# Kernel tuning notes

Hardware: AMD Instinct MI355X
Metric: run time of the kernel (lower is better)

The kernel has to match this reference:

```python
import jax, jax.numpy as jnp
import numpy as np

BATCH, DIN, DSTATE, SEQLEN = 4, 2048, 16, 2048


def setup_inputs() -> dict:
    key = jax.random.key(0)
    ks = jax.random.split(key, 7)
    u = jax.random.normal(ks[0], (BATCH, DIN, SEQLEN), dtype=jnp.float32)
    # delta pre-softplus; moderate positive-ish values like Mamba dt_proj output
    delta = jax.random.uniform(ks[1], (BATCH, DIN, SEQLEN), dtype=jnp.float32, minval=-2.0, maxval=1.0)
    # A is negative in real Mamba (A = -exp(A_log)); keep recurrence stable
    A = -jnp.exp(jax.random.uniform(ks[2], (DIN, DSTATE), dtype=jnp.float32, minval=-1.0, maxval=1.0))
    B = jax.random.normal(ks[3], (BATCH, DSTATE, SEQLEN), dtype=jnp.float32)
    C = jax.random.normal(ks[4], (BATCH, DSTATE, SEQLEN), dtype=jnp.float32)
    D = jax.random.normal(ks[5], (DIN,), dtype=jnp.float32)
    z = jax.random.normal(ks[6], (BATCH, DIN, SEQLEN), dtype=jnp.float32)
    return {"u": u, "delta": delta, "A": A, "B": B, "C": C, "D": D, "z": z}


def reference(u, delta, A, B, C, D, z):
    """Mamba selective scan (selective_scan_ref semantics, delta_softplus=True).

    u, delta, z: (b, d, l); A: (d, n); B, C: (b, n, l); D: (d,).
    y_t = C_t . x_t + D*u_t, x_t = exp(dt_t*A)*x_{t-1} + dt_t*B_t*u_t,
    final y gated by SiLU(z).
    """
    dt = jax.nn.softplus(delta)                      # (b, d, l)

    def step(x, inp):
        dt_t, u_t, B_t, C_t = inp                    # (b,d) (b,d) (b,n) (b,n)
        dA = jnp.exp(dt_t[..., None] * A)            # (b, d, n)
        x = x * dA + (dt_t * u_t)[..., None] * B_t[:, None, :]
        y_t = jnp.einsum('bdn,bn->bd', x, C_t)
        return x, y_t

    xs = (jnp.moveaxis(dt, -1, 0),                   # (l, b, d)
          jnp.moveaxis(u, -1, 0),
          jnp.moveaxis(B, -1, 0),                    # (l, b, n)
          jnp.moveaxis(C, -1, 0))
    x0 = jnp.zeros((u.shape[0], u.shape[1], A.shape[1]), dtype=u.dtype)
    _, ys = jax.lax.scan(step, x0, xs)               # ys: (l, b, d)
    y = jnp.moveaxis(ys, 0, -1)                      # (b, d, l)
    y = y + D[None, :, None] * u
    y = y * (z * jax.nn.sigmoid(z))                  # SiLU gate
    return y
```

## Files before the change

kernel.cpp:

```cpp
#include <hip/hip_runtime.h>


#define BATCHSZ 4
#define DIN 2048
#define NSTATE 16
#define SEQ 2048
#define NCH (BATCHSZ * DIN)
#define NGRP (NCH / 256)
#define TT 16
#define ST 20
#define L2E 1.44269504f

__device__ __forceinline__ float softplus_f(float v) {
    float e = __builtin_amdgcn_exp2f(v * L2E);
    return 0.69314718f * __builtin_amdgcn_logf(1.0f + e);
}

__device__ __forceinline__ float silu_f(float v) {
    float s = __builtin_amdgcn_rcpf(1.0f + __builtin_amdgcn_exp2f(-v * L2E));
    return v * s;
}

__device__ __forceinline__ float comp4(const float4& f, int k) {
    return k == 0 ? f.x : k == 1 ? f.y : k == 2 ? f.z : f.w;
}

__device__ __forceinline__ void set4(float4& f, int k, float v) {
    if (k == 0) f.x = v; else if (k == 1) f.y = v; else if (k == 2) f.z = v; else f.w = v;
}


template<int NC>
__global__ __launch_bounds__(256, 3) void k_pass1(
        const float* __restrict__ u, const float* __restrict__ delta,
        const float* __restrict__ A, const float* __restrict__ Bm,
        float* __restrict__ ws) {
    constexpr int LC = SEQ / NC;
    constexpr int NT = LC / TT;
    __shared__ float Ub[256 * ST];
    __shared__ float Db[256 * ST];
    __shared__ float Bc[LC * 20];

    int tid = threadIdx.x;
    int g = blockIdx.x & (NGRP - 1);
    int c = blockIdx.x >> 5;
    int chBase = g << 8;
    int b = chBase >> 11;
    int bd = chBase + tid;
    int d = bd & (DIN - 1);

    float A2[NSTATE];
    {
        const float* Ar = A + (size_t)d * NSTATE;
        #pragma unroll
        for (int n = 0; n < NSTATE; ++n) A2[n] = Ar[n] * L2E;
    }

    const float* ug = u + (size_t)chBase * SEQ + (size_t)c * LC;
    const float* dg = delta + (size_t)chBase * SEQ + (size_t)c * LC;
    const float* Bg = Bm + (size_t)b * NSTATE * SEQ + (size_t)c * LC;

    #pragma unroll
    for (int i = 0; i < LC * NSTATE / 256; ++i) {
        int e = i * 256 + tid;
        int n = e / LC;
        int t = e % LC;
        Bc[t * 20 + n] = Bg[(size_t)n * SEQ + t];
    }

    float x[NSTATE];
    #pragma unroll
    for (int n = 0; n < NSTATE; ++n) x[n] = 0.0f;
    float S = 0.0f;

    float4 uvr[4], dvr[4];
    #pragma unroll
    for (int it = 0; it < 4; ++it) {
        int r = it * 64 + (tid >> 2), cq = (tid & 3) * 4;
        uvr[it] = *(const float4*)(ug + (size_t)r * SEQ + cq);
        dvr[it] = *(const float4*)(dg + (size_t)r * SEQ + cq);
    }

    for (int tile = 0; tile < NT; ++tile) {
        int tb = tile * TT;
        __syncthreads();
        #pragma unroll
        for (int it = 0; it < 4; ++it) {
            int r = it * 64 + (tid >> 2), cq = (tid & 3) * 4;
            *(float4*)(&Ub[r * ST + cq]) = uvr[it];
            *(float4*)(&Db[r * ST + cq]) = dvr[it];
        }
        __syncthreads();
        if (tile + 1 < NT) {
            #pragma unroll
            for (int it = 0; it < 4; ++it) {
                int r = it * 64 + (tid >> 2), cq = (tid & 3) * 4;
                uvr[it] = *(const float4*)(ug + (size_t)r * SEQ + tb + TT + cq);
                dvr[it] = *(const float4*)(dg + (size_t)r * SEQ + tb + TT + cq);
            }
        }
        #pragma unroll
        for (int t4 = 0; t4 < TT / 4; ++t4) {
            float4 u4 = *(const float4*)(&Ub[tid * ST + t4 * 4]);
            float4 d4 = *(const float4*)(&Db[tid * ST + t4 * 4]);
            #pragma unroll
            for (int k = 0; k < 4; ++k) {
                float dt = softplus_f(comp4(d4, k));
                S += dt;
                float du = dt * comp4(u4, k);
                int t = tb + t4 * 4 + k;
                const float4* Br = (const float4*)(&Bc[t * 20]);
                float bb[NSTATE];
                *(float4*)&bb[0] = Br[0]; *(float4*)&bb[4] = Br[1];
                *(float4*)&bb[8] = Br[2]; *(float4*)&bb[12] = Br[3];
                #pragma unroll
                for (int n = 0; n < NSTATE; ++n) {
                    float dA = __builtin_amdgcn_exp2f(A2[n] * dt);
                    x[n] = x[n] * dA + du * bb[n];
                }
            }
        }
    }

    float* wsq = ws;
    float* wsS = ws + (size_t)NSTATE * NC * NCH;
    #pragma unroll
    for (int n = 0; n < NSTATE; ++n) wsq[((size_t)n * NC + c) * NCH + bd] = x[n];
    wsS[(size_t)c * NCH + bd] = S;
}

template<int NC>
__global__ __launch_bounds__(256) void k_pass2(
        const float* __restrict__ A, float* __restrict__ ws) {
    int idx = blockIdx.x * 256 + threadIdx.x;
    int n = idx >> 13;
    int bd = idx & (NCH - 1);
    int d = bd & (DIN - 1);

    float A2 = A[(size_t)d * NSTATE + n] * L2E;
    float x = 0.0f;
    float* wsq = ws;
    float* wsS = ws + (size_t)NSTATE * NC * NCH;

    for (int c = 0; c < NC; ++c) {
        float S = wsS[(size_t)c * NCH + bd];
        float* p = wsq + ((size_t)n * NC + c) * NCH + bd;
        float q = *p;
        float P = __builtin_amdgcn_exp2f(A2 * S);
        *p = x;
        x = x * P + q;
    }
}

template<int NC>
__global__ __launch_bounds__(256, 3) void k_pass3(
        const float* __restrict__ u, const float* __restrict__ delta,
        const float* __restrict__ A, const float* __restrict__ Bm,
        const float* __restrict__ Cm, const float* __restrict__ Dv,
        const float* __restrict__ z, const float* __restrict__ ws,
        float* __restrict__ out) {
    constexpr int LC = SEQ / NC;
    constexpr int NT = LC / TT;
    __shared__ float Ub[256 * ST];
    __shared__ float Db[256 * ST];
    __shared__ float Bc[LC * 20];
    __shared__ float Cc[LC * 20];

    int tid = threadIdx.x;
    int g = blockIdx.x & (NGRP - 1);
    int c = blockIdx.x >> 5;
    int chBase = g << 8;
    int b = chBase >> 11;
    int bd = chBase + tid;
    int d = bd & (DIN - 1);

    float A2[NSTATE];
    {
        const float* Ar = A + (size_t)d * NSTATE;
        #pragma unroll
        for (int n = 0; n < NSTATE; ++n) A2[n] = Ar[n] * L2E;
    }

    const float* ug = u + (size_t)chBase * SEQ + (size_t)c * LC;
    const float* dg = delta + (size_t)chBase * SEQ + (size_t)c * LC;
    const float* zg = z + (size_t)chBase * SEQ + (size_t)c * LC;
    float* og = out + (size_t)chBase * SEQ + (size_t)c * LC;
    const float* Bg = Bm + (size_t)b * NSTATE * SEQ + (size_t)c * LC;
    const float* Cg = Cm + (size_t)b * NSTATE * SEQ + (size_t)c * LC;

    #pragma unroll
    for (int i = 0; i < LC * NSTATE / 256; ++i) {
        int e = i * 256 + tid;
        int n = e / LC;
        int t = e % LC;
        Bc[t * 20 + n] = Bg[(size_t)n * SEQ + t];
        Cc[t * 20 + n] = Cg[(size_t)n * SEQ + t];
    }

    const float* wsq = ws;
    float x[NSTATE];
    #pragma unroll
    for (int n = 0; n < NSTATE; ++n)
        x[n] = wsq[((size_t)n * NC + c) * NCH + bd];
    float Dd = Dv[d];

    float4 uvr[4], dvr[4];
    #pragma unroll
    for (int it = 0; it < 4; ++it) {
        int r = it * 64 + (tid >> 2), cq = (tid & 3) * 4;
        uvr[it] = *(const float4*)(ug + (size_t)r * SEQ + cq);
        dvr[it] = *(const float4*)(dg + (size_t)r * SEQ + cq);
    }

    for (int tile = 0; tile < NT; ++tile) {
        int tb = tile * TT;
        __syncthreads();
        #pragma unroll
        for (int it = 0; it < 4; ++it) {
            int r = it * 64 + (tid >> 2), cq = (tid & 3) * 4;
            *(float4*)(&Ub[r * ST + cq]) = uvr[it];
            *(float4*)(&Db[r * ST + cq]) = dvr[it];
        }
        __syncthreads();
        if (tile + 1 < NT) {
            #pragma unroll
            for (int it = 0; it < 4; ++it) {
                int r = it * 64 + (tid >> 2), cq = (tid & 3) * 4;
                uvr[it] = *(const float4*)(ug + (size_t)r * SEQ + tb + TT + cq);
                dvr[it] = *(const float4*)(dg + (size_t)r * SEQ + tb + TT + cq);
            }
        }
        #pragma unroll
        for (int t4 = 0; t4 < TT / 4; ++t4) {
            float4 u4 = *(const float4*)(&Ub[tid * ST + t4 * 4]);
            float4 d4 = *(const float4*)(&Db[tid * ST + t4 * 4]);
            float4 y4;
            #pragma unroll
            for (int k = 0; k < 4; ++k) {
                float uv = comp4(u4, k);
                float dt = softplus_f(comp4(d4, k));
                float du = dt * uv;
                int t = tb + t4 * 4 + k;
                const float4* Br = (const float4*)(&Bc[t * 20]);
                const float4* Cr = (const float4*)(&Cc[t * 20]);
                float bb[NSTATE], cc[NSTATE];
                *(float4*)&bb[0] = Br[0]; *(float4*)&bb[4] = Br[1];
                *(float4*)&bb[8] = Br[2]; *(float4*)&bb[12] = Br[3];
                *(float4*)&cc[0] = Cr[0]; *(float4*)&cc[4] = Cr[1];
                *(float4*)&cc[8] = Cr[2]; *(float4*)&cc[12] = Cr[3];
                float acc = 0.0f;
                #pragma unroll
                for (int n = 0; n < NSTATE; ++n) {
                    float dA = __builtin_amdgcn_exp2f(A2[n] * dt);
                    x[n] = x[n] * dA + du * bb[n];
                    acc += x[n] * cc[n];
                }
                set4(y4, k, acc + Dd * uv);
            }
            *(float4*)(&Ub[tid * ST + t4 * 4]) = y4;
        }
        __syncthreads();
        #pragma unroll
        for (int it = 0; it < 4; ++it) {
            int r = it * 64 + (tid >> 2), cq = (tid & 3) * 4;
            float4 y4 = *(const float4*)(&Ub[r * ST + cq]);
            float4 z4 = *(const float4*)(zg + (size_t)r * SEQ + tb + cq);
            float4 oo;
            #pragma unroll
            for (int k = 0; k < 4; ++k)
                set4(oo, k, comp4(y4, k) * silu_f(comp4(z4, k)));
            *(float4*)(og + (size_t)r * SEQ + tb + cq) = oo;
        }
    }
}

__global__ __launch_bounds__(256) void k_simple(
        const float* __restrict__ u, const float* __restrict__ delta,
        const float* __restrict__ A, const float* __restrict__ Bm,
        const float* __restrict__ Cm, const float* __restrict__ Dv,
        const float* __restrict__ z, float* __restrict__ out) {
    int bd = blockIdx.x * 256 + threadIdx.x;
    int b  = bd >> 11;
    int d  = bd & (DIN - 1);

    float A2[NSTATE];
    const float* Ar = A + d * NSTATE;
    #pragma unroll
    for (int n = 0; n < NSTATE; ++n) A2[n] = Ar[n] * L2E;
    float x[NSTATE];
    #pragma unroll
    for (int n = 0; n < NSTATE; ++n) x[n] = 0.0f;

    float Dd = Dv[d];
    size_t base = (size_t)bd * SEQ;
    const float4* u4 = (const float4*)(u + base);
    const float4* d4 = (const float4*)(delta + base);
    const float4* z4 = (const float4*)(z + base);
    float4* o4 = (float4*)(out + base);
    const float* Bp = Bm + (size_t)b * NSTATE * SEQ;
    const float* Cp = Cm + (size_t)b * NSTATE * SEQ;

    for (int t4 = 0; t4 < SEQ / 4; ++t4) {
        float4 uu = u4[t4];
        float4 dd = d4[t4];
        float4 zz = z4[t4];
        float4 yy;
        #pragma unroll
        for (int k = 0; k < 4; ++k) {
            float uv = comp4(uu, k);
            float dt = softplus_f(comp4(dd, k));
            float du = dt * uv;
            int t = t4 * 4 + k;
            float acc = 0.0f;
            #pragma unroll
            for (int n = 0; n < NSTATE; ++n) {
                float dA = __builtin_amdgcn_exp2f(A2[n] * dt);
                x[n] = x[n] * dA + du * Bp[n * SEQ + t];
                acc += x[n] * Cp[n * SEQ + t];
            }
            float y = acc + Dd * uv;
            y = y * silu_f(comp4(zz, k));
            set4(yy, k, y);
        }
        o4[t4] = yy;
    }
}

template<int NC>
static void launch_chunked(const float* u, const float* delta, const float* A,
                           const float* Bm, const float* Cm, const float* Dv,
                           const float* z, float* ws, float* out, hipStream_t stream) {
    k_pass1<NC><<<NGRP * NC, 256, 0, stream>>>(u, delta, A, Bm, ws);
    k_pass2<NC><<<(NSTATE * NCH) / 256, 256, 0, stream>>>(A, ws);
    k_pass3<NC><<<NGRP * NC, 256, 0, stream>>>(u, delta, A, Bm, Cm, Dv, z, ws, out);
}

extern "C" void kernel_launch(void* const* d_in, const int* in_sizes, int n_in,
                              void* d_out, int out_size, void* d_ws, size_t ws_size,
                              hipStream_t stream) {
    const float* u     = (const float*)d_in[0];
    const float* delta = (const float*)d_in[1];
    const float* A     = (const float*)d_in[2];
    const float* Bm    = (const float*)d_in[3];
    const float* Cm    = (const float*)d_in[4];
    const float* Dv    = (const float*)d_in[5];
    const float* z     = (const float*)d_in[6];
    float* out = (float*)d_out;
    float* ws = (float*)d_ws;

    size_t need64 = (size_t)(NSTATE + 1) * 64 * NCH * sizeof(float);
    size_t need32 = (size_t)(NSTATE + 1) * 32 * NCH * sizeof(float);
    size_t need16 = (size_t)(NSTATE + 1) * 16 * NCH * sizeof(float);
    if (ws_size >= need64) {
        launch_chunked<64>(u, delta, A, Bm, Cm, Dv, z, ws, out, stream);
    } else if (ws_size >= need32) {
        launch_chunked<32>(u, delta, A, Bm, Cm, Dv, z, ws, out, stream);
    } else if (ws_size >= need16) {
        launch_chunked<16>(u, delta, A, Bm, Cm, Dv, z, ws, out, stream);
    } else {
        k_simple<<<NCH / 256, 256, 0, stream>>>(u, delta, A, Bm, Cm, Dv, z, out);
    }
}
```

Before: 445.0 us.

## Double time tile width, drop register prefetch, preload z before scan

Widens the time tile staged in shared memory from 16 to 32 steps (row stride 36) and lowers the occupancy hint from 3 to 2 blocks per SM in both the chunk-local scan and the output pass. The register-held prefetch of the next u/delta tile is removed; each tile is now loaded straight from global into LDS right before use. In the output pass, z for the tile is loaded into registers before the scan so its latency is hidden behind the compute. The aim is fewer barriers per sequence and lower register pressure, at the cost of no longer overlapping the next tile's u/delta loads with the current scan, plus larger LDS use and lower occupancy.

```diff
diff --git a/kernel.cpp b/kernel.cpp
--- a/kernel.cpp
+++ b/kernel.cpp
@@ -7,8 +7,8 @@
 #define SEQ 2048
 #define NCH (BATCHSZ * DIN)
 #define NGRP (NCH / 256)
-#define TT 16
-#define ST 20
+#define TT 32
+#define ST 36
 #define L2E 1.44269504f
 
 __device__ __forceinline__ float softplus_f(float v) {
@@ -31,7 +31,7 @@
 
 
 template<int NC>
-__global__ __launch_bounds__(256, 3) void k_pass1(
+__global__ __launch_bounds__(256, 2) void k_pass1(
         const float* __restrict__ u, const float* __restrict__ delta,
         const float* __restrict__ A, const float* __restrict__ Bm,
         float* __restrict__ ws) {
@@ -73,32 +73,16 @@
     for (int n = 0; n < NSTATE; ++n) x[n] = 0.0f;
     float S = 0.0f;
 
-    float4 uvr[4], dvr[4];
-    #pragma unroll
-    for (int it = 0; it < 4; ++it) {
-        int r = it * 64 + (tid >> 2), cq = (tid & 3) * 4;
-        uvr[it] = *(const float4*)(ug + (size_t)r * SEQ + cq);
-        dvr[it] = *(const float4*)(dg + (size_t)r * SEQ + cq);
-    }
-
     for (int tile = 0; tile < NT; ++tile) {
         int tb = tile * TT;
         __syncthreads();
         #pragma unroll
-        for (int it = 0; it < 4; ++it) {
-            int r = it * 64 + (tid >> 2), cq = (tid & 3) * 4;
-            *(float4*)(&Ub[r * ST + cq]) = uvr[it];
-            *(float4*)(&Db[r * ST + cq]) = dvr[it];
-        }
-        __syncthreads();
-        if (tile + 1 < NT) {
-            #pragma unroll
-            for (int it = 0; it < 4; ++it) {
-                int r = it * 64 + (tid >> 2), cq = (tid & 3) * 4;
-                uvr[it] = *(const float4*)(ug + (size_t)r * SEQ + tb + TT + cq);
-                dvr[it] = *(const float4*)(dg + (size_t)r * SEQ + tb + TT + cq);
-            }
-        }
+        for (int it = 0; it < 8; ++it) {
+            int r = it * 32 + (tid >> 3), cq = (tid & 7) * 4;
+            *(float4*)(&Ub[r * ST + cq]) = *(const float4*)(ug + (size_t)r * SEQ + tb + cq);
+            *(float4*)(&Db[r * ST + cq]) = *(const float4*)(dg + (size_t)r * SEQ + tb + cq);
+        }
+        __syncthreads();
         #pragma unroll
         for (int t4 = 0; t4 < TT / 4; ++t4) {
             float4 u4 = *(const float4*)(&Ub[tid * ST + t4 * 4]);
@@ -153,7 +137,7 @@
 }
 
 template<int NC>
-__global__ __launch_bounds__(256, 3) void k_pass3(
+__global__ __launch_bounds__(256, 2) void k_pass3(
         const float* __restrict__ u, const float* __restrict__ delta,
         const float* __restrict__ A, const float* __restrict__ Bm,
         const float* __restrict__ Cm, const float* __restrict__ Dv,
@@ -204,32 +188,18 @@
         x[n] = wsq[((size_t)n * NC + c) * NCH + bd];
     float Dd = Dv[d];
 
-    float4 uvr[4], dvr[4];
-    #pragma unroll
-    for (int it = 0; it < 4; ++it) {
-        int r = it * 64 + (tid >> 2), cq = (tid & 3) * 4;
-        uvr[it] = *(const float4*)(ug + (size_t)r * SEQ + cq);
-        dvr[it] = *(const float4*)(dg + (size_t)r * SEQ + cq);
-    }
-
     for (int tile = 0; tile < NT; ++tile) {
         int tb = tile * TT;
         __syncthreads();
-        #pragma unroll
-        for (int it = 0; it < 4; ++it) {
-            int r = it * 64 + (tid >> 2), cq = (tid & 3) * 4;
-            *(float4*)(&Ub[r * ST + cq]) = uvr[it];
-            *(float4*)(&Db[r * ST + cq]) = dvr[it];
-        }
-        __syncthreads();
-        if (tile + 1 < NT) {
-            #pragma unroll
-            for (int it = 0; it < 4; ++it) {
-                int r = it * 64 + (tid >> 2), cq = (tid & 3) * 4;
-                uvr[it] = *(const float4*)(ug + (size_t)r * SEQ + tb + TT + cq);
-                dvr[it] = *(const float4*)(dg + (size_t)r * SEQ + tb + TT + cq);
-            }
-        }
+        float4 zr[8];
+        #pragma unroll
+        for (int it = 0; it < 8; ++it) {
+            int r = it * 32 + (tid >> 3), cq = (tid & 7) * 4;
+            *(float4*)(&Ub[r * ST + cq]) = *(const float4*)(ug + (size_t)r * SEQ + tb + cq);
+            *(float4*)(&Db[r * ST + cq]) = *(const float4*)(dg + (size_t)r * SEQ + tb + cq);
+            zr[it] = *(const float4*)(zg + (size_t)r * SEQ + tb + cq);
+        }
+        __syncthreads();
         #pragma unroll
         for (int t4 = 0; t4 < TT / 4; ++t4) {
             float4 u4 = *(const float4*)(&Ub[tid * ST + t4 * 4]);
@@ -261,14 +231,13 @@
         }
         __syncthreads();
         #pragma unroll
-        for (int it = 0; it < 4; ++it) {
-            int r = it * 64 + (tid >> 2), cq = (tid & 3) * 4;
+        for (int it = 0; it < 8; ++it) {
+            int r = it * 32 + (tid >> 3), cq = (tid & 7) * 4;
             float4 y4 = *(const float4*)(&Ub[r * ST + cq]);
-            float4 z4 = *(const float4*)(zg + (size_t)r * SEQ + tb + cq);
             float4 oo;
             #pragma unroll
             for (int k = 0; k < 4; ++k)
-                set4(oo, k, comp4(y4, k) * silu_f(comp4(z4, k)));
+                set4(oo, k, comp4(y4, k) * silu_f(comp4(zr[it], k)));
             *(float4*)(og + (size_t)r * SEQ + tb + cq) = oo;
         }
     }
```

After: 377.9 us. 1.18x faster.
